# Optimization experiments

Measured on AMD Instinct MI355X. Metric: run time of the kernel, lower is better.

## Reference

```python
import jax, jax.numpy as jnp
import numpy as np


def _gcn_conv(x, edge_index, W, b):
    """Faithful PyG GCNConv: add self-loops, symmetric norm, scatter-sum, bias."""
    n = x.shape[0]
    loop = jnp.arange(n, dtype=edge_index.dtype)
    src = jnp.concatenate([edge_index[0], loop])  # [E+n]
    dst = jnp.concatenate([edge_index[1], loop])
    # in-degree at dst (edge_weight = 1), as in gcn_norm
    deg = jax.ops.segment_sum(jnp.ones(src.shape[0], x.dtype), dst, num_segments=n)
    dinv = jnp.where(deg > 0, jax.lax.rsqrt(deg), 0.0)
    norm = dinv[src] * dinv[dst]                  # [E+n]
    h = x @ W                                     # [n, C] small GEMM
    msg = h[src] * norm[:, None]                  # gather + scale (dominant traffic)
    out = jax.ops.segment_sum(msg, dst, num_segments=n)  # scatter-sum
    return out + b


def setup_inputs() -> dict:
    key = jax.random.key(0)
    ks = jax.random.split(key, 8)
    N, E, C = 50000, 1000000, 64
    scale = 1.0 / np.sqrt(C)
    return {
        "x_star": jax.random.normal(ks[0], (N, C), jnp.float32),
        "x_gal": jax.random.normal(ks[1], (N, C), jnp.float32),
        "edge_ss_near": jax.random.randint(ks[2], (2, E), 0, N, jnp.int64),
        "edge_ss_far": jax.random.randint(ks[3], (2, E), 0, N, jnp.int64),
        "edge_gg_near": jax.random.randint(ks[4], (2, E), 0, N, jnp.int64),
        "W_ss_near": jax.random.normal(ks[5], (C, C), jnp.float32) * scale,
        "W_ss_far": jax.random.normal(ks[6], (C, C), jnp.float32) * scale,
        "W_gg_near": jax.random.normal(ks[7], (C, C), jnp.float32) * scale,
        "b_ss_near": jnp.zeros((C,), jnp.float32),
        "b_ss_far": jnp.zeros((C,), jnp.float32),
        "b_gg_near": jnp.zeros((C,), jnp.float32),
    }


def reference(x_star, x_gal, edge_ss_near, edge_ss_far, edge_gg_near,
              W_ss_near, W_ss_far, W_gg_near,
              b_ss_near, b_ss_far, b_gg_near):
    # HeteroConv with aggr='sum': per-edge-type GCNConv, summed per dst node type.
    out_star = (_gcn_conv(x_star, edge_ss_near, W_ss_near, b_ss_near)
                + _gcn_conv(x_star, edge_ss_far, W_ss_far, b_ss_far))
    out_gal = _gcn_conv(x_gal, edge_gg_near, W_gg_near, b_gg_near)
    return out_star, out_gal
```

## Files before the change

kernel.cpp:

```cpp
#include <hip/hip_runtime.h>
#include <hip/hip_fp16.h>

#define CCH 64
#define RPB 32
#define PCH 8192
#define NBMAX 1568
#define GR 64
#define SG 8
#define STCAP 8192

typedef int int4a __attribute__((ext_vector_type(4), aligned(4)));

__global__ void __launch_bounds__(256) k_hist(const int* __restrict__ e0,
        const int* __restrict__ e1, const int* __restrict__ e2,
        int* __restrict__ H, int* __restrict__ cnt, int E, int NB, int NBLK) {
    int c = blockIdx.y;
    const int* dd = ((c == 0) ? e0 : (c == 1) ? e1 : e2) + E;
    int base = blockIdx.x * PCH;
    int nE = E - base; if (nE > PCH) nE = PCH;
    __shared__ int hist[NBMAX];
    int t = threadIdx.x;
    for (int i = t; i < NB; i += 256) hist[i] = 0;
    __syncthreads();
    for (int k = t * 4; k < nE; k += 1024) {
        if (k + 3 < nE) {
            int4a d = *(const int4a*)(dd + base + k);
            atomicAdd(&hist[d.x >> 5], 1); atomicAdd(&hist[d.y >> 5], 1);
            atomicAdd(&hist[d.z >> 5], 1); atomicAdd(&hist[d.w >> 5], 1);
        } else {
            for (int j = k; j < nE; ++j) atomicAdd(&hist[dd[base + j] >> 5], 1);
        }
    }
    __syncthreads();
    int* Hrow = H + ((size_t)c * NBLK + blockIdx.x) * NB;
    for (int i = t; i < NB; i += 256) {
        int h = hist[i];
        Hrow[i] = h;
        if (h) atomicAdd(&cnt[c * NB + i], h);
    }
}

__global__ void __launch_bounds__(1024) k_bscan(const int* __restrict__ cnt,
        int* __restrict__ bstart, int NB, int E) {
    int c = blockIdx.x, t = threadIdx.x;
    __shared__ int sm[1024];
    int i0 = 2 * t, i1 = 2 * t + 1;
    int v0 = (i0 < NB) ? cnt[c * NB + i0] : 0;
    int v1 = (i1 < NB) ? cnt[c * NB + i1] : 0;
    sm[t] = v0 + v1;
    __syncthreads();
    #pragma unroll
    for (int off = 1; off < 1024; off <<= 1) {
        int u = (t >= off) ? sm[t - off] : 0;
        __syncthreads();
        sm[t] += u;
        __syncthreads();
    }
    int ex = sm[t] - (v0 + v1);
    if (i0 < NB) bstart[c * (NB + 1) + i0] = ex;
    if (i1 < NB) bstart[c * (NB + 1) + i1] = ex + v0;
    if (t == 0) bstart[c * (NB + 1) + NB] = E;
}

__global__ void __launch_bounds__(256) k_colscan(int* __restrict__ H,
        const int* __restrict__ bstart, int NB, int NBLK) {
    int c = blockIdx.y;
    int b = blockIdx.x * 4 + (threadIdx.x >> 6);
    if (b >= NB) return;
    int l = threadIdx.x & 63;
    int* Hc = H + (size_t)c * NBLK * NB;
    int run = bstart[c * (NB + 1) + b];
    for (int c0 = 0; c0 < NBLK; c0 += 64) {
        int blk = c0 + l;
        int v = (blk < NBLK) ? Hc[(size_t)blk * NB + b] : 0;
        int s = v;
        #pragma unroll
        for (int off = 1; off < 64; off <<= 1) {
            int u = __shfl_up(s, off, 64);
            if (l >= off) s += u;
        }
        if (blk < NBLK) Hc[(size_t)blk * NB + b] = run + s - v;
        run += __shfl(s, 63, 64);
    }
}

__global__ void __launch_bounds__(256) k_part2(const int* __restrict__ e0,
        const int* __restrict__ e1, const int* __restrict__ e2,
        const int* __restrict__ H, unsigned* __restrict__ bdata,
        int E, int NB, int NBLK) {
    int c = blockIdx.y;
    const int* ed = (c == 0) ? e0 : (c == 1) ? e1 : e2;
    int base = blockIdx.x * PCH;
    int nE = E - base; if (nE > PCH) nE = PCH;
    __shared__ unsigned staged[PCH];
    __shared__ int hist[NBMAX];
    __shared__ int off[NBMAX];
    __shared__ int sm[256];
    int t = threadIdx.x;
    for (int i = t; i < NB; i += 256) hist[i] = 0;
    const int* Hrow = H + ((size_t)c * NBLK + blockIdx.x) * NB;
    for (int i = t; i < NB; i += 256) off[i] = Hrow[i];
    __syncthreads();
    for (int k = t * 4; k < nE; k += 1024) {
        if (k + 3 < nE) {
            int4a d = *(const int4a*)(ed + E + base + k);
            atomicAdd(&hist[d.x >> 5], 1); atomicAdd(&hist[d.y >> 5], 1);
            atomicAdd(&hist[d.z >> 5], 1); atomicAdd(&hist[d.w >> 5], 1);
        } else {
            for (int j = k; j < nE; ++j) atomicAdd(&hist[ed[E + base + j] >> 5], 1);
        }
    }
    __syncthreads();
    int C = (NB + 255) >> 8;
    int lo = t * C, hi = lo + C; if (hi > NB) hi = NB; if (lo > NB) lo = NB;
    int s = 0;
    for (int i = lo; i < hi; ++i) s += hist[i];
    sm[t] = s;
    __syncthreads();
    #pragma unroll
    for (int o = 1; o < 256; o <<= 1) {
        int u = (t >= o) ? sm[t - o] : 0;
        __syncthreads();
        sm[t] += u;
        __syncthreads();
    }
    int run = (t == 0) ? 0 : sm[t - 1];
    for (int i = lo; i < hi; ++i) {
        int h = hist[i];
        off[i] -= run;
        hist[i] = run;
        run += h;
    }
    __syncthreads();
    for (int k = t * 4; k < nE; k += 1024) {
        if (k + 3 < nE) {
            int4a s4 = *(const int4a*)(ed + base + k);
            int4a d4 = *(const int4a*)(ed + E + base + k);
            int sl;
            sl = atomicAdd(&hist[d4.x >> 5], 1); staged[sl] = (unsigned)s4.x | ((unsigned)d4.x << 16);
            sl = atomicAdd(&hist[d4.y >> 5], 1); staged[sl] = (unsigned)s4.y | ((unsigned)d4.y << 16);
            sl = atomicAdd(&hist[d4.z >> 5], 1); staged[sl] = (unsigned)s4.z | ((unsigned)d4.z << 16);
            sl = atomicAdd(&hist[d4.w >> 5], 1); staged[sl] = (unsigned)s4.w | ((unsigned)d4.w << 16);
        } else {
            for (int j = k; j < nE; ++j) {
                int s0 = ed[base + j];
                int d0 = ed[E + base + j];
                int sl = atomicAdd(&hist[d0 >> 5], 1);
                staged[sl] = (unsigned)s0 | ((unsigned)d0 << 16);
            }
        }
    }
    __syncthreads();
    unsigned* bo = bdata + (size_t)c * E;
    for (int sI = t; sI < nE; sI += 256) {
        unsigned rec = staged[sI];
        int b = (int)(rec >> 16) >> 5;
        bo[off[b] + sI] = rec;
    }
}

__global__ void __launch_bounds__(256) k_sort32(const unsigned* __restrict__ bdata,
        const int* __restrict__ bstart, int* __restrict__ sdat,
        int* __restrict__ rs, float* __restrict__ dinv, int E, int N, int NB) {
    int c = blockIdx.y;
    int b0 = blockIdx.x * SG;
    __shared__ unsigned staged[STCAP];
    __shared__ int cnt[SG * RPB];
    __shared__ int cur[SG * RPB];
    __shared__ int sb[SG + 1];
    int t = threadIdx.x;
    cnt[t] = 0;
    if (t <= SG) {
        int b = b0 + t; if (b > NB) b = NB;
        sb[t] = bstart[c * (NB + 1) + b];
    }
    __syncthreads();
    int s0 = sb[0], sE = sb[SG];
    int n = sE - s0;
    const unsigned* bd = bdata + (size_t)c * E;
    bool fits = (n <= STCAP);
    if (fits) {
        for (int i = t; i < n; i += 256) staged[i] = bd[s0 + i];
        __syncthreads();
        for (int i = t; i < n; i += 256) {
            int dst = (int)(staged[i] >> 16);
            atomicAdd(&cnt[((dst >> 5) - b0) * RPB + (dst & 31)], 1);
        }
    } else {
        for (int i = s0 + t; i < sE; i += 256) {
            int dst = (int)(bd[i] >> 16);
            atomicAdd(&cnt[((dst >> 5) - b0) * RPB + (dst & 31)], 1);
        }
    }
    __syncthreads();
    {
        int v = cnt[t];
        int s = v;
        #pragma unroll
        for (int off = 1; off < RPB; off <<= 1) {
            int u = __shfl_up(s, off, RPB);
            if ((t & (RPB - 1)) >= off) s += u;
        }
        int g = t >> 5, r = t & 31;
        int ex = sb[g] + s - v;
        cur[t] = ex;
        int row = (b0 + g) * RPB + r;
        if (b0 + g < NB && row < N) {
            rs[c * (N + 1) + row] = ex;
            dinv[c * N + row] = rsqrtf((float)(v + 1));
        }
    }
    if (blockIdx.x == 0 && t == 0) rs[c * (N + 1) + N] = E;
    __syncthreads();
    int* so = sdat + (size_t)c * E;
    if (fits) {
        for (int i = t; i < n; i += 256) {
            unsigned r = staged[i];
            int dst = (int)(r >> 16);
            int slot = atomicAdd(&cur[((dst >> 5) - b0) * RPB + (dst & 31)], 1);
            so[slot] = (int)(r & 0xFFFFu);
        }
    } else {
        for (int i = s0 + t; i < sE; i += 256) {
            unsigned r = bd[i];
            int dst = (int)(r >> 16);
            int slot = atomicAdd(&cur[((dst >> 5) - b0) * RPB + (dst & 31)], 1);
            so[slot] = (int)(r & 0xFFFFu);
        }
    }
}

__global__ void __launch_bounds__(256) k_gemm_all(const float* __restrict__ xs_,
        const float* __restrict__ xg_, const float* __restrict__ W0,
        const float* __restrict__ W1, const float* __restrict__ W2,
        const float* __restrict__ dinv, __half* __restrict__ h16, int N) {
    int c = blockIdx.y;
    const float* x = (c == 2) ? xg_ : xs_;
    const float* W = (c == 0) ? W0 : (c == 1) ? W1 : W2;
    __shared__ float Ws[CCH * CCH];
    __shared__ float xT[CCH * (GR + 1)];
    int t = threadIdx.x;
    int row0 = blockIdx.x * GR;
    #pragma unroll
    for (int j = 0; j < 4; ++j) {
        int idx = j * 1024 + t * 4;
        *(float4*)(Ws + idx) = *(const float4*)(W + idx);
    }
    #pragma unroll
    for (int j = 0; j < 4; ++j) {
        int idx = t + j * 256;
        int r = idx >> 4;
        int c0 = (idx & 15) * 4;
        int row = row0 + r;
        float4 v = make_float4(0.f, 0.f, 0.f, 0.f);
        if (row < N) v = *(const float4*)(x + (size_t)row * CCH + c0);
        xT[(c0 + 0) * (GR + 1) + r] = v.x;
        xT[(c0 + 1) * (GR + 1) + r] = v.y;
        xT[(c0 + 2) * (GR + 1) + r] = v.z;
        xT[(c0 + 3) * (GR + 1) + r] = v.w;
    }
    __syncthreads();
    int c4 = (t & 15) * 4;
    int r0 = (t >> 4) * 4;
    float4 a0 = make_float4(0.f, 0.f, 0.f, 0.f), a1 = a0, a2 = a0, a3 = a0;
    #pragma unroll 8
    for (int k = 0; k < CCH; ++k) {
        float4 wv = *(float4*)(Ws + k * CCH + c4);
        float x0 = xT[k * (GR + 1) + r0 + 0];
        float x1 = xT[k * (GR + 1) + r0 + 1];
        float x2 = xT[k * (GR + 1) + r0 + 2];
        float x3 = xT[k * (GR + 1) + r0 + 3];
        a0.x += x0 * wv.x; a0.y += x0 * wv.y; a0.z += x0 * wv.z; a0.w += x0 * wv.w;
        a1.x += x1 * wv.x; a1.y += x1 * wv.y; a1.z += x1 * wv.z; a1.w += x1 * wv.w;
        a2.x += x2 * wv.x; a2.y += x2 * wv.y; a2.z += x2 * wv.z; a2.w += x2 * wv.w;
        a3.x += x3 * wv.x; a3.y += x3 * wv.y; a3.z += x3 * wv.z; a3.w += x3 * wv.w;
    }
    const float* dv = dinv + c * N;
    __half* hc = h16 + (size_t)c * N * CCH;
    float4 av[4] = {a0, a1, a2, a3};
    #pragma unroll
    for (int i = 0; i < 4; ++i) {
        int row = row0 + r0 + i;
        if (row < N) {
            float dd = dv[row];
            union { __half2 h2[2]; float2 f2; } u;
            u.h2[0] = __floats2half2_rn(av[i].x * dd, av[i].y * dd);
            u.h2[1] = __floats2half2_rn(av[i].z * dd, av[i].w * dd);
            *(float2*)(hc + (size_t)row * CCH + c4) = u.f2;
        }
    }
}

__device__ __forceinline__ float4 gat4(const __half* __restrict__ hc, int s, int l16) {
    union { float2 f2; __half2 h2[2]; } u;
    u.f2 = ((const float2*)(hc + (size_t)s * CCH))[l16];
    float2 a = __half22float2(u.h2[0]);
    float2 b = __half22float2(u.h2[1]);
    return make_float4(a.x, a.y, b.x, b.y);
}

__device__ __forceinline__ void acc4(float4& a, float4 v) {
    a.x += v.x; a.y += v.y; a.z += v.z; a.w += v.w;
}

__global__ void __launch_bounds__(256) k_pull(const int* __restrict__ rs,
        const int* __restrict__ sdat, const __half* __restrict__ h16,
        const float* __restrict__ dinv,
        const float* __restrict__ b0, const float* __restrict__ b1,
        const float* __restrict__ b2,
        float* __restrict__ out, int N, int E) {
    int row = blockIdx.x * 4 + (threadIdx.x >> 6);
    if (row >= 2 * N) return;
    int lane = threadIdx.x & 63;
    int q = lane >> 4;
    int l16 = lane & 15;
    size_t NC = (size_t)N * CCH;

    const __half* hcL;
    const int* sdL;
    int beg, end;
    float ddL;
    float4 bias;
    float* op;
    float4 acc = make_float4(0.f, 0.f, 0.f, 0.f);
    if (row < N) {
        int cv = q >> 1;
        const int* rsA = rs + cv * (N + 1);
        int bg = rsA[row], eg = rsA[row + 1];
        int mid = (bg + eg) >> 1;
        beg = (q & 1) ? mid : bg;
        end = (q & 1) ? eg : mid;
        hcL = h16 + (size_t)cv * NC;
        sdL = sdat + (size_t)cv * E;
        ddL = dinv[cv * N + row];
        if (!(q & 1)) acc = gat4(hcL, row, l16);
        float4 bv0 = ((const float4*)b0)[l16];
        float4 bv1 = ((const float4*)b1)[l16];
        bias = make_float4(bv0.x + bv1.x, bv0.y + bv1.y,
                           bv0.z + bv1.z, bv0.w + bv1.w);
        op = out + (size_t)row * CCH;
    } else {
        int r = row - N;
        const int* rs2 = rs + 2 * (N + 1);
        int bg = rs2[r], eg = rs2[r + 1];
        int len = eg - bg;
        beg = bg + ((len * q) >> 2);
        end = bg + ((len * (q + 1)) >> 2);
        hcL = h16 + 2 * NC;
        sdL = sdat + 2 * (size_t)E;
        ddL = dinv[2 * N + r];
        if (q == 0) acc = gat4(hcL, r, l16);
        bias = ((const float4*)b2)[l16];
        op = out + NC + (size_t)r * CCH;
    }

    int i = beg;
    for (; i + 7 < end; i += 8) {
        int4a q0 = *(const int4a*)(sdL + i);
        int4a q1 = *(const int4a*)(sdL + i + 4);
        float4 v0 = gat4(hcL, q0.x, l16);
        float4 v1 = gat4(hcL, q0.y, l16);
        float4 v2 = gat4(hcL, q0.z, l16);
        float4 v3 = gat4(hcL, q0.w, l16);
        float4 v4 = gat4(hcL, q1.x, l16);
        float4 v5 = gat4(hcL, q1.y, l16);
        float4 v6 = gat4(hcL, q1.z, l16);
        float4 v7 = gat4(hcL, q1.w, l16);
        acc4(acc, v0); acc4(acc, v1); acc4(acc, v2); acc4(acc, v3);
        acc4(acc, v4); acc4(acc, v5); acc4(acc, v6); acc4(acc, v7);
    }
    for (; i + 3 < end; i += 4) {
        int4a q0 = *(const int4a*)(sdL + i);
        float4 v0 = gat4(hcL, q0.x, l16);
        float4 v1 = gat4(hcL, q0.y, l16);
        float4 v2 = gat4(hcL, q0.z, l16);
        float4 v3 = gat4(hcL, q0.w, l16);
        acc4(acc, v0); acc4(acc, v1); acc4(acc, v2); acc4(acc, v3);
    }
    for (; i < end; ++i) acc4(acc, gat4(hcL, sdL[i], l16));

    float4 t;
    t.x = acc.x * ddL; t.y = acc.y * ddL; t.z = acc.z * ddL; t.w = acc.w * ddL;
    t.x += __shfl_xor(t.x, 16, 64); t.y += __shfl_xor(t.y, 16, 64);
    t.z += __shfl_xor(t.z, 16, 64); t.w += __shfl_xor(t.w, 16, 64);
    t.x += __shfl_xor(t.x, 32, 64); t.y += __shfl_xor(t.y, 32, 64);
    t.z += __shfl_xor(t.z, 32, 64); t.w += __shfl_xor(t.w, 32, 64);
    if (lane < 16) {
        t.x += bias.x; t.y += bias.y; t.z += bias.z; t.w += bias.w;
        ((float4*)op)[l16] = t;
    }
}

static inline size_t align256(size_t x) { return (x + 255) & ~(size_t)255; }

extern "C" void kernel_launch(void* const* d_in, const int* in_sizes, int n_in,
                              void* d_out, int out_size, void* d_ws, size_t ws_size,
                              hipStream_t stream) {
    const float* x_star = (const float*)d_in[0];
    const float* x_gal  = (const float*)d_in[1];
    const int*   e_ssn  = (const int*)d_in[2];
    const int*   e_ssf  = (const int*)d_in[3];
    const int*   e_ggn  = (const int*)d_in[4];
    const float* W_ssn  = (const float*)d_in[5];
    const float* W_ssf  = (const float*)d_in[6];
    const float* W_ggn  = (const float*)d_in[7];
    const float* b_ssn  = (const float*)d_in[8];
    const float* b_ssf  = (const float*)d_in[9];
    const float* b_ggn  = (const float*)d_in[10];

    const int N  = in_sizes[0] / CCH;
    const int E  = in_sizes[2] / 2;
    const size_t NC = (size_t)N * CCH;
    const int NB   = (N + RPB - 1) / RPB;
    const int NBLK = (E + PCH - 1) / PCH;

    char* w = (char*)d_ws;
    __half*   h16    = (__half*)w;   w += align256((size_t)3 * NC * 2);
    float*    dinv   = (float*)w;    w += align256((size_t)3 * N * 4);
    unsigned* bdata  = (unsigned*)w; w += align256((size_t)3 * E * 4);
    int*      sdat   = (int*)w;      w += align256((size_t)3 * E * 4);
    int*      H      = (int*)w;      w += align256((size_t)3 * NBLK * NB * 4);
    int*      cnt    = (int*)w;      w += align256((size_t)3 * NB * 4);
    int*      bstart = (int*)w;      w += align256((size_t)3 * (NB + 1) * 4);
    int*      rs     = (int*)w;      w += align256((size_t)3 * (N + 1) * 4);

    const int B = 256;

    hipMemsetAsync(cnt, 0, (size_t)3 * NB * 4, stream);
    k_hist<<<dim3(NBLK, 3), B, 0, stream>>>(e_ssn, e_ssf, e_ggn, H, cnt, E, NB, NBLK);
    k_bscan<<<3, 1024, 0, stream>>>(cnt, bstart, NB, E);
    k_colscan<<<dim3((NB + 3) / 4, 3), B, 0, stream>>>(H, bstart, NB, NBLK);
    k_part2<<<dim3(NBLK, 3), B, 0, stream>>>(e_ssn, e_ssf, e_ggn, H, bdata, E, NB, NBLK);
    k_sort32<<<dim3((NB + SG - 1) / SG, 3), B, 0, stream>>>(bdata, bstart, sdat,
                                                            rs, dinv, E, N, NB);
    k_gemm_all<<<dim3((N + GR - 1) / GR, 3), B, 0, stream>>>(x_star, x_gal,
                                                             W_ssn, W_ssf, W_ggn,
                                                             dinv, h16, N);
    k_pull<<<(2 * N + 3) / 4, B, 0, stream>>>(rs, sdat, h16, dinv,
                                              b_ssn, b_ssf, b_ggn,
                                              (float*)d_out, N, E);
}
```

Before: 244.6 us.

## Derive partition histogram from scanned offsets and widen pull gather to sixteen

The partition kernel no longer re-reads destination indices to rebuild its per-block bucket histogram with shared atomics. It recovers the counts as differences between consecutive rows of the already column-scanned offset table, using the bucket starts for the last block. The pull kernel replaces its 8/4/1 unrolled loops with one 16-wide loop. Slots past the segment end point at a zeroed row instead of branching, which raises loads in flight but issues wasted loads on short segments. Source indices are masked to 16 bits, which assumes the node count stays below 65536.

```diff
diff --git a/kernel.cpp b/kernel.cpp
--- a/kernel.cpp
+++ b/kernel.cpp
@@ -86,8 +86,8 @@
 
 __global__ void __launch_bounds__(256) k_part2(const int* __restrict__ e0,
         const int* __restrict__ e1, const int* __restrict__ e2,
-        const int* __restrict__ H, unsigned* __restrict__ bdata,
-        int E, int NB, int NBLK) {
+        const int* __restrict__ H, const int* __restrict__ bstart,
+        unsigned* __restrict__ bdata, int E, int NB, int NBLK) {
     int c = blockIdx.y;
     const int* ed = (c == 0) ? e0 : (c == 1) ? e1 : e2;
     int base = blockIdx.x * PCH;
@@ -97,18 +97,13 @@
     __shared__ int off[NBMAX];
     __shared__ int sm[256];
     int t = threadIdx.x;
-    for (int i = t; i < NB; i += 256) hist[i] = 0;
-    const int* Hrow = H + ((size_t)c * NBLK + blockIdx.x) * NB;
-    for (int i = t; i < NB; i += 256) off[i] = Hrow[i];
-    __syncthreads();
-    for (int k = t * 4; k < nE; k += 1024) {
-        if (k + 3 < nE) {
-            int4a d = *(const int4a*)(ed + E + base + k);
-            atomicAdd(&hist[d.x >> 5], 1); atomicAdd(&hist[d.y >> 5], 1);
-            atomicAdd(&hist[d.z >> 5], 1); atomicAdd(&hist[d.w >> 5], 1);
-        } else {
-            for (int j = k; j < nE; ++j) atomicAdd(&hist[ed[E + base + j] >> 5], 1);
-        }
+    const int* Hcur = H + ((size_t)c * NBLK + blockIdx.x) * NB;
+    const int* Hnxt = (blockIdx.x == NBLK - 1) ? (bstart + c * (NB + 1) + 1)
+                                               : (Hcur + NB);
+    for (int i = t; i < NB; i += 256) {
+        int cu = Hcur[i];
+        off[i] = cu;
+        hist[i] = Hnxt[i] - cu;
     }
     __syncthreads();
     int C = (NB + 255) >> 8;
@@ -291,9 +286,9 @@
     }
 }
 
-__device__ __forceinline__ float4 gat4(const __half* __restrict__ hc, int s, int l16) {
+__device__ __forceinline__ float4 gat4p(const __half* __restrict__ p, int l16) {
     union { float2 f2; __half2 h2[2]; } u;
-    u.f2 = ((const float2*)(hc + (size_t)s * CCH))[l16];
+    u.f2 = ((const float2*)p)[l16];
     float2 a = __half22float2(u.h2[0]);
     float2 b = __half22float2(u.h2[1]);
     return make_float4(a.x, a.y, b.x, b.y);
@@ -305,7 +300,7 @@
 
 __global__ void __launch_bounds__(256) k_pull(const int* __restrict__ rs,
         const int* __restrict__ sdat, const __half* __restrict__ h16,
-        const float* __restrict__ dinv,
+        const float* __restrict__ dinv, const __half* __restrict__ zrow,
         const float* __restrict__ b0, const float* __restrict__ b1,
         const float* __restrict__ b2,
         float* __restrict__ out, int N, int E) {
@@ -333,7 +328,7 @@
         hcL = h16 + (size_t)cv * NC;
         sdL = sdat + (size_t)cv * E;
         ddL = dinv[cv * N + row];
-        if (!(q & 1)) acc = gat4(hcL, row, l16);
+        if (!(q & 1)) acc = gat4p(hcL + (size_t)row * CCH, l16);
         float4 bv0 = ((const float4*)b0)[l16];
         float4 bv1 = ((const float4*)b1)[l16];
         bias = make_float4(bv0.x + bv1.x, bv0.y + bv1.y,
@@ -349,35 +344,53 @@
         hcL = h16 + 2 * NC;
         sdL = sdat + 2 * (size_t)E;
         ddL = dinv[2 * N + r];
-        if (q == 0) acc = gat4(hcL, r, l16);
+        if (q == 0) acc = gat4p(hcL + (size_t)r * CCH, l16);
         bias = ((const float4*)b2)[l16];
         op = out + NC + (size_t)r * CCH;
     }
 
-    int i = beg;
-    for (; i + 7 < end; i += 8) {
+    for (int i = beg; i < end; i += 16) {
         int4a q0 = *(const int4a*)(sdL + i);
         int4a q1 = *(const int4a*)(sdL + i + 4);
-        float4 v0 = gat4(hcL, q0.x, l16);
-        float4 v1 = gat4(hcL, q0.y, l16);
-        float4 v2 = gat4(hcL, q0.z, l16);
-        float4 v3 = gat4(hcL, q0.w, l16);
-        float4 v4 = gat4(hcL, q1.x, l16);
-        float4 v5 = gat4(hcL, q1.y, l16);
-        float4 v6 = gat4(hcL, q1.z, l16);
-        float4 v7 = gat4(hcL, q1.w, l16);
-        acc4(acc, v0); acc4(acc, v1); acc4(acc, v2); acc4(acc, v3);
-        acc4(acc, v4); acc4(acc, v5); acc4(acc, v6); acc4(acc, v7);
-    }
-    for (; i + 3 < end; i += 4) {
-        int4a q0 = *(const int4a*)(sdL + i);
-        float4 v0 = gat4(hcL, q0.x, l16);
-        float4 v1 = gat4(hcL, q0.y, l16);
-        float4 v2 = gat4(hcL, q0.z, l16);
-        float4 v3 = gat4(hcL, q0.w, l16);
-        acc4(acc, v0); acc4(acc, v1); acc4(acc, v2); acc4(acc, v3);
-    }
-    for (; i < end; ++i) acc4(acc, gat4(hcL, sdL[i], l16));
+        int4a q2 = *(const int4a*)(sdL + i + 8);
+        int4a q3 = *(const int4a*)(sdL + i + 12);
+        const __half* p0  = hcL + (size_t)(q0.x & 0xFFFF) * CCH;
+        const __half* p1  = (i + 1  < end) ? hcL + (size_t)(q0.y & 0xFFFF) * CCH : zrow;
+        const __half* p2  = (i + 2  < end) ? hcL + (size_t)(q0.z & 0xFFFF) * CCH : zrow;
+        const __half* p3  = (i + 3  < end) ? hcL + (size_t)(q0.w & 0xFFFF) * CCH : zrow;
+        const __half* p4  = (i + 4  < end) ? hcL + (size_t)(q1.x & 0xFFFF) * CCH : zrow;
+        const __half* p5  = (i + 5  < end) ? hcL + (size_t)(q1.y & 0xFFFF) * CCH : zrow;
+        const __half* p6  = (i + 6  < end) ? hcL + (size_t)(q1.z & 0xFFFF) * CCH : zrow;
+        const __half* p7  = (i + 7  < end) ? hcL + (size_t)(q1.w & 0xFFFF) * CCH : zrow;
+        const __half* p8  = (i + 8  < end) ? hcL + (size_t)(q2.x & 0xFFFF) * CCH : zrow;
+        const __half* p9  = (i + 9  < end) ? hcL + (size_t)(q2.y & 0xFFFF) * CCH : zrow;
+        const __half* p10 = (i + 10 < end) ? hcL + (size_t)(q2.z & 0xFFFF) * CCH : zrow;
+        const __half* p11 = (i + 11 < end) ? hcL + (size_t)(q2.w & 0xFFFF) * CCH : zrow;
+        const __half* p12 = (i + 12 < end) ? hcL + (size_t)(q3.x & 0xFFFF) * CCH : zrow;
+        const __half* p13 = (i + 13 < end) ? hcL + (size_t)(q3.y & 0xFFFF) * CCH : zrow;
+        const __half* p14 = (i + 14 < end) ? hcL + (size_t)(q3.z & 0xFFFF) * CCH : zrow;
+        const __half* p15 = (i + 15 < end) ? hcL + (size_t)(q3.w & 0xFFFF) * CCH : zrow;
+        float4 v0  = gat4p(p0,  l16);
+        float4 v1  = gat4p(p1,  l16);
+        float4 v2  = gat4p(p2,  l16);
+        float4 v3  = gat4p(p3,  l16);
+        float4 v4  = gat4p(p4,  l16);
+        float4 v5  = gat4p(p5,  l16);
+        float4 v6  = gat4p(p6,  l16);
+        float4 v7  = gat4p(p7,  l16);
+        float4 v8  = gat4p(p8,  l16);
+        float4 v9  = gat4p(p9,  l16);
+        float4 v10 = gat4p(p10, l16);
+        float4 v11 = gat4p(p11, l16);
+        float4 v12 = gat4p(p12, l16);
+        float4 v13 = gat4p(p13, l16);
+        float4 v14 = gat4p(p14, l16);
+        float4 v15 = gat4p(p15, l16);
+        acc4(acc, v0);  acc4(acc, v1);  acc4(acc, v2);  acc4(acc, v3);
+        acc4(acc, v4);  acc4(acc, v5);  acc4(acc, v6);  acc4(acc, v7);
+        acc4(acc, v8);  acc4(acc, v9);  acc4(acc, v10); acc4(acc, v11);
+        acc4(acc, v12); acc4(acc, v13); acc4(acc, v14); acc4(acc, v15);
+    }
 
     float4 t;
     t.x = acc.x * ddL; t.y = acc.y * ddL; t.z = acc.z * ddL; t.w = acc.w * ddL;
@@ -423,20 +436,23 @@
     int*      cnt    = (int*)w;      w += align256((size_t)3 * NB * 4);
     int*      bstart = (int*)w;      w += align256((size_t)3 * (NB + 1) * 4);
     int*      rs     = (int*)w;      w += align256((size_t)3 * (N + 1) * 4);
+    __half*   zrow   = (__half*)w;   w += align256((size_t)CCH * 2);
 
     const int B = 256;
 
     hipMemsetAsync(cnt, 0, (size_t)3 * NB * 4, stream);
+    hipMemsetAsync(zrow, 0, (size_t)CCH * 2, stream);
     k_hist<<<dim3(NBLK, 3), B, 0, stream>>>(e_ssn, e_ssf, e_ggn, H, cnt, E, NB, NBLK);
     k_bscan<<<3, 1024, 0, stream>>>(cnt, bstart, NB, E);
     k_colscan<<<dim3((NB + 3) / 4, 3), B, 0, stream>>>(H, bstart, NB, NBLK);
-    k_part2<<<dim3(NBLK, 3), B, 0, stream>>>(e_ssn, e_ssf, e_ggn, H, bdata, E, NB, NBLK);
+    k_part2<<<dim3(NBLK, 3), B, 0, stream>>>(e_ssn, e_ssf, e_ggn, H, bstart,
+                                             bdata, E, NB, NBLK);
     k_sort32<<<dim3((NB + SG - 1) / SG, 3), B, 0, stream>>>(bdata, bstart, sdat,
                                                             rs, dinv, E, N, NB);
     k_gemm_all<<<dim3((N + GR - 1) / GR, 3), B, 0, stream>>>(x_star, x_gal,
                                                              W_ssn, W_ssf, W_ggn,
                                                              dinv, h16, N);
-    k_pull<<<(2 * N + 3) / 4, B, 0, stream>>>(rs, sdat, h16, dinv,
+    k_pull<<<(2 * N + 3) / 4, B, 0, stream>>>(rs, sdat, h16, dinv, zrow,
                                               b_ssn, b_ssf, b_ggn,
                                               (float*)d_out, N, E);
 }
```

New measurement: 252.0 us. +3.0%, slower.
